# Kernel tuning notes

Measured on AMD Instinct MI355X. Metric: run time of the kernel, lower is better.

Reference implementation:

```python
import jax, jax.numpy as jnp
import numpy as np

N = 50000      # nodes
E = 800000     # edges
IN, HID, OUT = 256, 64, 64
H1, H2 = 4, 1
NEG_SLOPE = 0.2  # DGL GATConv default


def gat_layer(x, W, a_l, a_r, b, src, dst, n_heads, d_out, activation=None):
    # x: [N, F_in]; W: [F_in, n_heads*d_out]; a_l/a_r: [n_heads, d_out]; b: [n_heads*d_out]
    z = (x @ W).reshape(N, n_heads, d_out)                      # [N,H,D]
    el = jnp.sum(z * a_l[None], axis=-1)                        # [N,H] score from src side
    er = jnp.sum(z * a_r[None], axis=-1)                        # [N,H] score from dst side
    e = jax.nn.leaky_relu(el[src] + er[dst], NEG_SLOPE)         # [E,H]
    # edge-softmax normalized over incoming edges of each dst node
    m = jax.ops.segment_max(e, dst, num_segments=N)             # [N,H]
    ex = jnp.exp(e - m[dst])                                    # [E,H]
    s = jax.ops.segment_sum(ex, dst, num_segments=N)            # [N,H]
    alpha = ex / s[dst]                                         # [E,H]
    # scatter-weighted aggregation of neighbor (src) features
    msg = alpha[:, :, None] * z[src]                            # [E,H,D]
    out = jax.ops.segment_sum(msg, dst, num_segments=N)         # [N,H,D]
    out = out + b.reshape(1, n_heads, d_out)
    if activation is not None:
        out = activation(out)
    return out


def setup_inputs() -> dict:
    key = jax.random.key(0)
    ks = jax.random.split(key, 12)
    x = jax.random.normal(ks[0], (N, IN), dtype=jnp.float32)
    src = jax.random.randint(ks[1], (E,), 0, N, dtype=jnp.int32)
    dst = jax.random.randint(ks[2], (E,), 0, N, dtype=jnp.int32)
    sc1 = 1.0 / np.sqrt(IN)
    sc2 = 1.0 / np.sqrt(HID * H1)
    W1 = jax.random.normal(ks[3], (IN, H1 * HID), dtype=jnp.float32) * sc1
    al1 = jax.random.normal(ks[4], (H1, HID), dtype=jnp.float32) * 0.1
    ar1 = jax.random.normal(ks[5], (H1, HID), dtype=jnp.float32) * 0.1
    b1 = jnp.zeros((H1 * HID,), dtype=jnp.float32)
    W2 = jax.random.normal(ks[6], (HID * H1, H2 * OUT), dtype=jnp.float32) * sc2
    al2 = jax.random.normal(ks[7], (H2, OUT), dtype=jnp.float32) * 0.1
    ar2 = jax.random.normal(ks[8], (H2, OUT), dtype=jnp.float32) * 0.1
    b2 = jnp.zeros((H2 * OUT,), dtype=jnp.float32)
    return {"x": x, "W1": W1, "al1": al1, "ar1": ar1, "b1": b1,
            "W2": W2, "al2": al2, "ar2": ar2, "b2": b2,
            "src": src, "dst": dst}


def reference(x, W1, al1, ar1, b1, W2, al2, ar2, b2, src, dst):
    # layer 1: GATConv(IN -> HID, H1 heads), elu activation, then flatten heads
    h = gat_layer(x, W1, al1, ar1, b1, src, dst, H1, HID, activation=jax.nn.elu)
    h = h.reshape(N, H1 * HID)
    # layer 2: GATConv(HID*H1 -> OUT, H2 heads), no activation, mean over heads
    h = gat_layer(h, W2, al2, ar2, b2, src, dst, H2, OUT, activation=None)
    return h.mean(axis=1)  # [N, OUT]
```

## Files before the change

### kernel.cpp

```cpp
#include <hip/hip_runtime.h>
#include <hip/hip_bf16.h>
#include <math.h>

#define NN 50000
#define EE 800000
#define FIN 256
#define HID 64
#define OUTD 64
#define H1 4
#define H2 1

typedef __attribute__((ext_vector_type(8))) short short8;
typedef __attribute__((ext_vector_type(4))) short short4v;
typedef __attribute__((ext_vector_type(4))) float f32x4;
typedef __attribute__((ext_vector_type(2))) float f32x2;


__device__ __forceinline__ unsigned short f2bf(float f) {
    unsigned u = __float_as_uint(f);
    unsigned r = (u + 0x7FFFu + ((u >> 16) & 1u)) >> 16;
    return (unsigned short)r;
}
__device__ __forceinline__ float bf2f(unsigned short u) {
    return __uint_as_float(((unsigned)u) << 16);
}


__global__ void hist_kernel(const int* __restrict__ dst, int* __restrict__ deg, int nE) {
    int e = blockIdx.x * 256 + threadIdx.x;
    if (e < nE) atomicAdd(&deg[dst[e]], 1);
}

__global__ void scan_block(const int* __restrict__ in, int* __restrict__ out,
                           int* __restrict__ bsums, int n) {
    __shared__ int sh[256];
    int i = blockIdx.x * 256 + threadIdx.x;
    int v = (i < n) ? in[i] : 0;
    sh[threadIdx.x] = v;
    __syncthreads();
    for (int off = 1; off < 256; off <<= 1) {
        int t = 0;
        if (threadIdx.x >= off) t = sh[threadIdx.x - off];
        __syncthreads();
        if (threadIdx.x >= off) sh[threadIdx.x] += t;
        __syncthreads();
    }
    if (i < n) out[i] = sh[threadIdx.x] - v;
    if (threadIdx.x == 255) bsums[blockIdx.x] = sh[255];
}

__global__ void scan_bsums(int* __restrict__ bsums, int nb) {
    __shared__ int sh[256];
    int v = (threadIdx.x < nb) ? bsums[threadIdx.x] : 0;
    sh[threadIdx.x] = v;
    __syncthreads();
    for (int off = 1; off < 256; off <<= 1) {
        int t = 0;
        if (threadIdx.x >= off) t = sh[threadIdx.x - off];
        __syncthreads();
        if (threadIdx.x >= off) sh[threadIdx.x] += t;
        __syncthreads();
    }
    if (threadIdx.x < nb) bsums[threadIdx.x] = sh[threadIdx.x] - v;
}

__global__ void add_offsets(int* __restrict__ out, const int* __restrict__ bsums,
                            int n, int Etot) {
    int i = blockIdx.x * 256 + threadIdx.x;
    if (i < n) out[i] += bsums[blockIdx.x];
    if (i == 0) out[n] = Etot;
}

__global__ void fill_csr(const int* __restrict__ src, const int* __restrict__ dst,
                         const int* __restrict__ rowptr, int* __restrict__ fillc,
                         int* __restrict__ csr_src, int nE) {
    int e = blockIdx.x * 256 + threadIdx.x;
    if (e < nE) {
        int d = dst[e];
        int pos = rowptr[d] + atomicAdd(&fillc[d], 1);
        csr_src[pos] = src[e];
    }
}


__global__ void wsplit(const float* __restrict__ W1, const float* __restrict__ W2,
                       short* __restrict__ W1th, short* __restrict__ W1tl,
                       short* __restrict__ W2th, short* __restrict__ W2tl) {
    int n = blockIdx.x;
    int k = threadIdx.x;
    if (n < 256) {
        float v = W1[(size_t)k * 256 + n];
        unsigned short hi = f2bf(v);
        unsigned short lo = f2bf(v - bf2f(hi));
        W1th[n * 256 + k] = (short)hi;
        W1tl[n * 256 + k] = (short)lo;
    } else {
        int n2 = n - 256;
        float v = W2[(size_t)k * 64 + n2];
        unsigned short hi = f2bf(v);
        unsigned short lo = f2bf(v - bf2f(hi));
        W2th[n2 * 256 + k] = (short)hi;
        W2tl[n2 * 256 + k] = (short)lo;
    }
}


template<int MF, int WR, int WC, int NT, int H, bool ASPLIT>
__global__ __launch_bounds__(256) void gemm_bf16x2(
    const void* __restrict__ Av, const short* __restrict__ Bth, const short* __restrict__ Btl,
    const float* __restrict__ al, const float* __restrict__ ar,
    unsigned short* __restrict__ zb, float* __restrict__ el, float* __restrict__ er,
    int M, int K)
{
    constexpr int BM = WR * MF * 16;
    constexpr int BN = WC * 64;
    __shared__ short Ah[BM * 40];
    __shared__ short Al[ASPLIT ? BM * 40 : 8];
    __shared__ short Bh[BN * 40], Bl[BN * 40];

    const int bm = blockIdx.x * BM;
    const int bn = blockIdx.y * BN;
    const int t = threadIdx.x;
    const int wid = t >> 6;
    const int lane = t & 63;
    const int lr = lane & 15;
    const int lg = lane >> 4;
    const int wr = wid / WC;
    const int wc = wid % WC;

    f32x4 acc[MF][4];
#pragma unroll
    for (int mf = 0; mf < MF; ++mf)
#pragma unroll
        for (int nf = 0; nf < 4; ++nf) acc[mf][nf] = (f32x4)(0.f);

    for (int k0 = 0; k0 < K; k0 += 32) {
        if constexpr (ASPLIT) {
            const float* A = (const float*)Av;
#pragma unroll
            for (int q = 0; q < BM / 32; ++q) {
                int linear = q * 256 + t;
                int row = linear >> 3;
                int kq = (linear & 7) * 4;
                int grow = bm + row;
                float4 av = make_float4(0.f, 0.f, 0.f, 0.f);
                if (grow < M) av = *(const float4*)(A + (size_t)grow * K + k0 + kq);
                short4v hi, lo;
                unsigned short h0 = f2bf(av.x); hi.x = (short)h0; lo.x = (short)f2bf(av.x - bf2f(h0));
                unsigned short h1v = f2bf(av.y); hi.y = (short)h1v; lo.y = (short)f2bf(av.y - bf2f(h1v));
                unsigned short h2v = f2bf(av.z); hi.z = (short)h2v; lo.z = (short)f2bf(av.z - bf2f(h2v));
                unsigned short h3v = f2bf(av.w); hi.w = (short)h3v; lo.w = (short)f2bf(av.w - bf2f(h3v));
                *(short4v*)&Ah[row * 40 + kq] = hi;
                *(short4v*)&Al[row * 40 + kq] = lo;
            }
        } else {
            const unsigned short* A = (const unsigned short*)Av;
#pragma unroll
            for (int q = 0; q < BM / 64; ++q) {
                int linear = q * 256 + t;
                int row = linear >> 2;
                int k8 = (linear & 3) * 8;
                int grow = bm + row;
                short8 v = (short8)(0);
                if (grow < M) v = *(const short8*)(A + (size_t)grow * K + k0 + k8);
                *(short8*)&Ah[row * 40 + k8] = v;
            }
        }
#pragma unroll
        for (int q = 0; q < BN / 64; ++q) {
            int linear = q * 256 + t;
            int n = linear >> 2;
            int k8 = (linear & 3) * 8;
            short8 vh = *(const short8*)(Bth + (size_t)(bn + n) * K + k0 + k8);
            short8 vl = *(const short8*)(Btl + (size_t)(bn + n) * K + k0 + k8);
            *(short8*)&Bh[n * 40 + k8] = vh;
            *(short8*)&Bl[n * 40 + k8] = vl;
        }
        __syncthreads();

        short8 ah[MF], alo[MF], bh[4], blo[4];
#pragma unroll
        for (int mf = 0; mf < MF; ++mf) {
            int row = wr * MF * 16 + mf * 16 + lr;
            ah[mf] = *(const short8*)&Ah[row * 40 + lg * 8];
            if constexpr (ASPLIT) alo[mf] = *(const short8*)&Al[row * 40 + lg * 8];
        }
#pragma unroll
        for (int nf = 0; nf < 4; ++nf) {
            int col = wc * 64 + nf * 16 + lr;
            bh[nf]  = *(const short8*)&Bh[col * 40 + lg * 8];
            blo[nf] = *(const short8*)&Bl[col * 40 + lg * 8];
        }
#pragma unroll
        for (int mf = 0; mf < MF; ++mf)
#pragma unroll
            for (int nf = 0; nf < 4; ++nf) {
                acc[mf][nf] = __builtin_amdgcn_mfma_f32_16x16x32_bf16(ah[mf], bh[nf],  acc[mf][nf], 0, 0, 0);
                acc[mf][nf] = __builtin_amdgcn_mfma_f32_16x16x32_bf16(ah[mf], blo[nf], acc[mf][nf], 0, 0, 0);
                if constexpr (ASPLIT)
                    acc[mf][nf] = __builtin_amdgcn_mfma_f32_16x16x32_bf16(alo[mf], bh[nf], acc[mf][nf], 0, 0, 0);
            }
        __syncthreads();
    }

    const int h = (bn + wc * 64) >> 6;
    float alv[4], arv[4];
#pragma unroll
    for (int nf = 0; nf < 4; ++nf) {
        alv[nf] = al[h * 64 + nf * 16 + lr];
        arv[nf] = ar[h * 64 + nf * 16 + lr];
    }
#pragma unroll
    for (int mf = 0; mf < MF; ++mf) {
#pragma unroll
        for (int j = 0; j < 4; ++j) {
            int row = bm + wr * MF * 16 + mf * 16 + lg * 4 + j;
            float sel = 0.f, ser = 0.f;
#pragma unroll
            for (int nf = 0; nf < 4; ++nf) {
                float v = acc[mf][nf][j];
                sel += v * alv[nf];
                ser += v * arv[nf];
                if (row < M)
                    zb[(size_t)row * NT + bn + wc * 64 + nf * 16 + lr] = f2bf(v);
            }
#pragma unroll
            for (int off = 1; off <= 8; off <<= 1) {
                sel += __shfl_xor(sel, off);
                ser += __shfl_xor(ser, off);
            }
            if (lr == 0 && row < M) {
                el[(size_t)row * H + h] = sel;
                er[(size_t)row * H + h] = ser;
            }
        }
    }
}


__global__ __launch_bounds__(256) void gat_aggregate_h4(
    const unsigned short* __restrict__ zb,
    const float* __restrict__ el,
    const float* __restrict__ er,
    const int* __restrict__ rowptr, const int* __restrict__ csr_src,
    const float* __restrict__ bias,
    unsigned short* __restrict__ out,
    int Nn)
{
    __shared__ float p_lds[4][64][4];
    __shared__ int   s_lds[4][64];
    int wid = threadIdx.x >> 6;
    int lane = threadIdx.x & 63;
    int n = blockIdx.x * 4 + wid;
    if (n >= Nn) return;
    int start = rowptr[n], end = rowptr[n + 1];
    int deg = end - start;
    float4 er4 = *(const float4*)(er + (size_t)n * 4);
    int hsel = lane >> 4;
    const unsigned lb = (unsigned)(lane << 3);

    f32x2 acc01 = {0.f, 0.f}, acc23 = {0.f, 0.f};
    float4 ssum = make_float4(0.f, 0.f, 0.f, 0.f);
    float m = -INFINITY;

    for (int c0 = 0; c0 < deg; c0 += 64) {
        int nc = min(64, deg - c0);
        int s_l = 0;
        float4 e4 = make_float4(-INFINITY, -INFINITY, -INFINITY, -INFINITY);
        float emax_l = -INFINITY;
        if (lane < nc) {
            s_l = csr_src[start + c0 + lane];
            float4 el4 = *(const float4*)(el + (size_t)s_l * 4);
            e4.x = el4.x + er4.x; e4.x = e4.x > 0.f ? e4.x : 0.2f * e4.x;
            e4.y = el4.y + er4.y; e4.y = e4.y > 0.f ? e4.y : 0.2f * e4.y;
            e4.z = el4.z + er4.z; e4.z = e4.z > 0.f ? e4.z : 0.2f * e4.z;
            e4.w = el4.w + er4.w; e4.w = e4.w > 0.f ? e4.w : 0.2f * e4.w;
            emax_l = fmaxf(fmaxf(e4.x, e4.y), fmaxf(e4.z, e4.w));
        }
        float cm = emax_l;
#pragma unroll
        for (int off = 32; off; off >>= 1) cm = fmaxf(cm, __shfl_xor(cm, off));
        float newm = fmaxf(m, cm);
        float scale = __expf(m - newm);
        ssum.x *= scale; ssum.y *= scale; ssum.z *= scale; ssum.w *= scale;
        f32x2 sc2 = {scale, scale};
        acc01 *= sc2; acc23 *= sc2;
        m = newm;
        float4 p4 = make_float4(0.f, 0.f, 0.f, 0.f);
        if (lane < nc) {
            p4.x = __expf(e4.x - m);
            p4.y = __expf(e4.y - m);
            p4.z = __expf(e4.z - m);
            p4.w = __expf(e4.w - m);
        }
        float4 cs = p4;
#pragma unroll
        for (int off = 32; off; off >>= 1) {
            cs.x += __shfl_xor(cs.x, off);
            cs.y += __shfl_xor(cs.y, off);
            cs.z += __shfl_xor(cs.z, off);
            cs.w += __shfl_xor(cs.w, off);
        }
        ssum.x += cs.x; ssum.y += cs.y; ssum.z += cs.z; ssum.w += cs.w;
        *(float4*)&p_lds[wid][lane][0] = p4;
        s_lds[wid][lane] = s_l;

        for (int tt = 0; tt < nc; tt += 8) {
            float w[8]; unsigned off32[8];
#pragma unroll
            for (int j = 0; j < 8; ++j) {
                int idx = tt + j;
                int ic = idx < nc ? idx : 0;
                w[j] = idx < nc ? p_lds[wid][ic][hsel] : 0.f;
                off32[j] = ((unsigned)s_lds[wid][ic] << 9) + lb;
            }
            uint2 u[8];
#pragma unroll
            for (int j = 0; j < 8; ++j)
                u[j] = *(const uint2*)((const char*)zb + off32[j]);
#pragma unroll
            for (int j = 0; j < 8; ++j) {
                f32x2 v01, v23, ww = {w[j], w[j]};
                v01.x = __uint_as_float(u[j].x << 16);
                v01.y = __uint_as_float(u[j].x & 0xffff0000u);
                v23.x = __uint_as_float(u[j].y << 16);
                v23.y = __uint_as_float(u[j].y & 0xffff0000u);
                acc01 = __builtin_elementwise_fma(ww, v01, acc01);
                acc23 = __builtin_elementwise_fma(ww, v23, acc23);
            }
        }
    }
    float4 acc = make_float4(acc01.x, acc01.y, acc23.x, acc23.y);
#pragma unroll
    for (int off = 16; off <= 32; off <<= 1) { }
    float s_h = hsel == 0 ? ssum.x : hsel == 1 ? ssum.y : hsel == 2 ? ssum.z : ssum.w;
    float inv = s_h > 0.f ? 1.f / s_h : 0.f;
    float4 b4 = *(const float4*)(bias + lane * 4);
    float ox = acc.x * inv + b4.x; ox = ox > 0.f ? ox : expm1f(ox);
    float oy = acc.y * inv + b4.y; oy = oy > 0.f ? oy : expm1f(oy);
    float oz = acc.z * inv + b4.z; oz = oz > 0.f ? oz : expm1f(oz);
    float ow = acc.w * inv + b4.w; ow = ow > 0.f ? ow : expm1f(ow);
    ushort4 o;
    o.x = f2bf(ox); o.y = f2bf(oy); o.z = f2bf(oz); o.w = f2bf(ow);
    *(ushort4*)(out + (size_t)n * 256 + lane * 4) = o;
}


__global__ void gat_aggregate_bf(const unsigned short* __restrict__ zb,
                                 const float* __restrict__ el, const float* __restrict__ er,
                                 const int* __restrict__ rowptr, const int* __restrict__ csr_src,
                                 const float* __restrict__ bias,
                                 float* __restrict__ out, int Nn)
{
    int gw = (blockIdx.x * blockDim.x + threadIdx.x) >> 6;
    int lane = threadIdx.x & 63;
    int n = gw;
    if (n >= Nn) return;
    int start = rowptr[n], end = rowptr[n + 1];
    int deg = end - start;
    float ern = er[n];

    int group = lane >> 4;
    int gl = lane & 15;
    const unsigned lb = (unsigned)(gl << 3);

    f32x2 acc01 = {0.f, 0.f}, acc23 = {0.f, 0.f};
    float m = -INFINITY;
    float ssum = 0.f;

    for (int c0 = 0; c0 < deg; c0 += 64) {
        int nc = min(64, deg - c0);
        int s_l = 0;
        float e_l = -INFINITY;
        if (lane < nc) {
            s_l = csr_src[start + c0 + lane];
            float e = el[s_l] + ern;
            e_l = e > 0.f ? e : 0.2f * e;
        }
        float cm = e_l;
#pragma unroll
        for (int off = 32; off; off >>= 1) cm = fmaxf(cm, __shfl_xor(cm, off));
        float newm = fmaxf(m, cm);
        float scale = __expf(m - newm);
        ssum *= scale;
        f32x2 sc2 = {scale, scale};
        acc01 *= sc2; acc23 *= sc2;
        m = newm;
        float p_l = (lane < nc) ? __expf(e_l - m) : 0.f;
        float cs = p_l;
#pragma unroll
        for (int off = 32; off; off >>= 1) cs += __shfl_xor(cs, off);
        ssum += cs;

        int nIter = (nc + 3) >> 2;
        for (int i0 = 0; i0 < nIter; i0 += 4) {
            float w[4]; unsigned off32[4];
#pragma unroll
            for (int j = 0; j < 4; ++j) {
                int tt = group + 4 * (i0 + j);
                int tc = tt & 63;
                float wv = __shfl(p_l, tc);
                int s = __shfl(s_l, tc);
                w[j] = (tt < nc) ? wv : 0.f;
                off32[j] = ((unsigned)s << 7) + lb;
            }
            uint2 u[4];
#pragma unroll
            for (int j = 0; j < 4; ++j)
                u[j] = *(const uint2*)((const char*)zb + off32[j]);
#pragma unroll
            for (int j = 0; j < 4; ++j) {
                f32x2 v01, v23, ww = {w[j], w[j]};
                v01.x = __uint_as_float(u[j].x << 16);
                v01.y = __uint_as_float(u[j].x & 0xffff0000u);
                v23.x = __uint_as_float(u[j].y << 16);
                v23.y = __uint_as_float(u[j].y & 0xffff0000u);
                acc01 = __builtin_elementwise_fma(ww, v01, acc01);
                acc23 = __builtin_elementwise_fma(ww, v23, acc23);
            }
        }
    }
    float4 acc = make_float4(acc01.x, acc01.y, acc23.x, acc23.y);
#pragma unroll
    for (int off = 16; off <= 32; off <<= 1) {
        acc.x += __shfl_xor(acc.x, off);
        acc.y += __shfl_xor(acc.y, off);
        acc.z += __shfl_xor(acc.z, off);
        acc.w += __shfl_xor(acc.w, off);
    }
    float inv = ssum > 0.f ? 1.f / ssum : 0.f;
    if (lane < 16) {
        float4 o;
        o.x = acc.x * inv + bias[gl * 4 + 0];
        o.y = acc.y * inv + bias[gl * 4 + 1];
        o.z = acc.z * inv + bias[gl * 4 + 2];
        o.w = acc.w * inv + bias[gl * 4 + 3];
        *(float4*)(out + (size_t)n * 64 + gl * 4) = o;
    }
}


static inline size_t align_up(size_t x, size_t a) { return (x + a - 1) & ~(a - 1); }

extern "C" void kernel_launch(void* const* d_in, const int* in_sizes, int n_in,
                              void* d_out, int out_size, void* d_ws, size_t ws_size,
                              hipStream_t stream) {
    const float* x   = (const float*)d_in[0];
    const float* W1  = (const float*)d_in[1];
    const float* al1 = (const float*)d_in[2];
    const float* ar1 = (const float*)d_in[3];
    const float* b1  = (const float*)d_in[4];
    const float* W2  = (const float*)d_in[5];
    const float* al2 = (const float*)d_in[6];
    const float* ar2 = (const float*)d_in[7];
    const float* b2  = (const float*)d_in[8];
    const int*   src = (const int*)d_in[9];
    const int*   dst = (const int*)d_in[10];
    float* out = (float*)d_out;

    char* ws = (char*)d_ws;
    size_t off = 0;
    unsigned short* zb1 = (unsigned short*)(ws + off); off = align_up(off + (size_t)NN * 256 * 2, 256);
    unsigned short* h1b = (unsigned short*)(ws + off); off = align_up(off + (size_t)NN * 256 * 2, 256);
    unsigned short* zb2 = (unsigned short*)(ws + off); off = align_up(off + (size_t)NN * 64 * 2, 256);
    float* el1 = (float*)(ws + off); off = align_up(off + (size_t)NN * H1 * 4, 256);
    float* er1 = (float*)(ws + off); off = align_up(off + (size_t)NN * H1 * 4, 256);
    float* el2 = (float*)(ws + off); off = align_up(off + (size_t)NN * 4, 256);
    float* er2 = (float*)(ws + off); off = align_up(off + (size_t)NN * 4, 256);
    short* W1th = (short*)(ws + off); off = align_up(off + 256 * 256 * 2, 256);
    short* W1tl = (short*)(ws + off); off = align_up(off + 256 * 256 * 2, 256);
    short* W2th = (short*)(ws + off); off = align_up(off + 64 * 256 * 2, 256);
    short* W2tl = (short*)(ws + off); off = align_up(off + 64 * 256 * 2, 256);
    int* rowptr = (int*)(ws + off); off = align_up(off + (size_t)(NN + 1) * 4, 256);
    int* deg    = (int*)(ws + off); off = align_up(off + (size_t)NN * 4, 256);
    int* fillc  = (int*)(ws + off); off = align_up(off + (size_t)NN * 4, 256);
    int* bsums  = (int*)(ws + off); off = align_up(off + 256 * 4, 256);
    int* csr_src = (int*)(ws + off); off = align_up(off + (size_t)EE * 4, 256);

    const int nScanBlocks = (NN + 255) / 256;
    const int nEdgeBlocks = (EE + 255) / 256;
    const int nMBlocks64 = (NN + 63) / 64;
    const int nMBlocks128 = (NN + 127) / 128;

    hipMemsetAsync(deg, 0, (size_t)NN * 4, stream);
    hipMemsetAsync(fillc, 0, (size_t)NN * 4, stream);
    wsplit<<<320, 256, 0, stream>>>(W1, W2, W1th, W1tl, W2th, W2tl);
    hist_kernel<<<nEdgeBlocks, 256, 0, stream>>>(dst, deg, EE);
    scan_block<<<nScanBlocks, 256, 0, stream>>>(deg, rowptr, bsums, NN);
    scan_bsums<<<1, 256, 0, stream>>>(bsums, nScanBlocks);
    add_offsets<<<nScanBlocks, 256, 0, stream>>>(rowptr, bsums, NN, EE);
    fill_csr<<<nEdgeBlocks, 256, 0, stream>>>(src, dst, rowptr, fillc, csr_src, EE);

    gemm_bf16x2<4, 1, 4, 256, 4, true><<<dim3(nMBlocks64, 1), 256, 0, stream>>>(
        x, W1th, W1tl, al1, ar1, zb1, el1, er1, NN, FIN);
    gat_aggregate_h4<<<(NN + 3) / 4, 256, 0, stream>>>(
        zb1, el1, er1, rowptr, csr_src, b1, h1b, NN);

    gemm_bf16x2<2, 4, 1, 64, 1, false><<<dim3(nMBlocks128, 1), 256, 0, stream>>>(
        h1b, W2th, W2tl, al2, ar2, zb2, el2, er2, NN, H1 * HID);
    gat_aggregate_bf<<<(NN * 64 + 255) / 256, 256, 0, stream>>>(
        zb2, el2, er2, rowptr, csr_src, b2, out, NN);
}
```

Baseline: 244.4 us.

## Fuse weight split into histogram, single-block scan, and enlarge layer-1 GEMM tile

Merges the weight bf16 hi/lo split into the edge-degree histogram kernel and replaces the three-kernel block scan with one 1024-thread single-block scan, cutting the number of launches in CSR construction. The layer-1 GEMM tile grows from 64 to 128 rows per block, and A fragments are loaded inside the mf loop so more rows fit without keeping every fragment live in registers. The single-block scan serialises 50k elements onto one CU, and the bigger GEMM tile halves the block count and may raise register pressure.

```diff
diff --git a/kernel.cpp b/kernel.cpp
--- a/kernel.cpp
+++ b/kernel.cpp
@@ -26,49 +26,67 @@
 }
 
 
-__global__ void hist_kernel(const int* __restrict__ dst, int* __restrict__ deg, int nE) {
+__global__ void hist_wsplit(const int* __restrict__ dst, int* __restrict__ deg, int nE,
+                            const float* __restrict__ W1, const float* __restrict__ W2,
+                            short* __restrict__ W1th, short* __restrict__ W1tl,
+                            short* __restrict__ W2th, short* __restrict__ W2tl) {
     int e = blockIdx.x * 256 + threadIdx.x;
     if (e < nE) atomicAdd(&deg[dst[e]], 1);
-}
-
-__global__ void scan_block(const int* __restrict__ in, int* __restrict__ out,
-                           int* __restrict__ bsums, int n) {
-    __shared__ int sh[256];
-    int i = blockIdx.x * 256 + threadIdx.x;
-    int v = (i < n) ? in[i] : 0;
-    sh[threadIdx.x] = v;
+    int n = blockIdx.x;
+    int k = threadIdx.x;
+    if (n < 256) {
+        float v = W1[(size_t)k * 256 + n];
+        unsigned short hi = f2bf(v);
+        unsigned short lo = f2bf(v - bf2f(hi));
+        W1th[n * 256 + k] = (short)hi;
+        W1tl[n * 256 + k] = (short)lo;
+    } else if (n < 320) {
+        int n2 = n - 256;
+        float v = W2[(size_t)k * 64 + n2];
+        unsigned short hi = f2bf(v);
+        unsigned short lo = f2bf(v - bf2f(hi));
+        W2th[n2 * 256 + k] = (short)hi;
+        W2tl[n2 * 256 + k] = (short)lo;
+    }
+}
+
+#define SCAN_CH 49
+__global__ __launch_bounds__(1024) void scan_one(const int* __restrict__ deg,
+                                                 int* __restrict__ rowptr) {
+    __shared__ int wsum[16];
+    int tid = threadIdx.x;
+    int lane = tid & 63;
+    int base = tid * SCAN_CH;
+    int loc[SCAN_CH];
+    int tot = 0;
+#pragma unroll
+    for (int j = 0; j < SCAN_CH; ++j) {
+        int idx = base + j;
+        int v = (idx < NN) ? deg[idx] : 0;
+        loc[j] = tot;
+        tot += v;
+    }
+    int incl = tot;
+#pragma unroll
+    for (int off = 1; off < 64; off <<= 1) {
+        int t = __shfl_up(incl, off);
+        if (lane >= off) incl += t;
+    }
+    if (lane == 63) wsum[tid >> 6] = incl;
     __syncthreads();
-    for (int off = 1; off < 256; off <<= 1) {
-        int t = 0;
-        if (threadIdx.x >= off) t = sh[threadIdx.x - off];
-        __syncthreads();
-        if (threadIdx.x >= off) sh[threadIdx.x] += t;
-        __syncthreads();
-    }
-    if (i < n) out[i] = sh[threadIdx.x] - v;
-    if (threadIdx.x == 255) bsums[blockIdx.x] = sh[255];
-}
-
-__global__ void scan_bsums(int* __restrict__ bsums, int nb) {
-    __shared__ int sh[256];
-    int v = (threadIdx.x < nb) ? bsums[threadIdx.x] : 0;
-    sh[threadIdx.x] = v;
+    if (tid == 0) {
+        int run = 0;
+#pragma unroll
+        for (int i = 0; i < 16; ++i) { int t = wsum[i]; wsum[i] = run; run += t; }
+    }
     __syncthreads();
-    for (int off = 1; off < 256; off <<= 1) {
-        int t = 0;
-        if (threadIdx.x >= off) t = sh[threadIdx.x - off];
-        __syncthreads();
-        if (threadIdx.x >= off) sh[threadIdx.x] += t;
-        __syncthreads();
-    }
-    if (threadIdx.x < nb) bsums[threadIdx.x] = sh[threadIdx.x] - v;
-}
-
-__global__ void add_offsets(int* __restrict__ out, const int* __restrict__ bsums,
-                            int n, int Etot) {
-    int i = blockIdx.x * 256 + threadIdx.x;
-    if (i < n) out[i] += bsums[blockIdx.x];
-    if (i == 0) out[n] = Etot;
+    int excl = wsum[tid >> 6] + incl - tot;
+#pragma unroll
+    for (int j = 0; j < SCAN_CH; ++j) {
+        int idx = base + j;
+        if (idx < NN) rowptr[idx] = excl + loc[j];
+    }
+    if (tid == 0) rowptr[NN] = EE;
 }
 
 __global__ void fill_csr(const int* __restrict__ src, const int* __restrict__ dst,
@@ -79,28 +97,6 @@
         int d = dst[e];
         int pos = rowptr[d] + atomicAdd(&fillc[d], 1);
         csr_src[pos] = src[e];
-    }
-}
-
-
-__global__ void wsplit(const float* __restrict__ W1, const float* __restrict__ W2,
-                       short* __restrict__ W1th, short* __restrict__ W1tl,
-                       short* __restrict__ W2th, short* __restrict__ W2tl) {
-    int n = blockIdx.x;
-    int k = threadIdx.x;
-    if (n < 256) {
-        float v = W1[(size_t)k * 256 + n];
-        unsigned short hi = f2bf(v);
-        unsigned short lo = f2bf(v - bf2f(hi));
-        W1th[n * 256 + k] = (short)hi;
-        W1tl[n * 256 + k] = (short)lo;
-    } else {
-        int n2 = n - 256;
-        float v = W2[(size_t)k * 64 + n2];
-        unsigned short hi = f2bf(v);
-        unsigned short lo = f2bf(v - bf2f(hi));
-        W2th[n2 * 256 + k] = (short)hi;
-        W2tl[n2 * 256 + k] = (short)lo;
     }
 }
 
@@ -178,13 +174,7 @@
         }
         __syncthreads();
 
-        short8 ah[MF], alo[MF], bh[4], blo[4];
-#pragma unroll
-        for (int mf = 0; mf < MF; ++mf) {
-            int row = wr * MF * 16 + mf * 16 + lr;
-            ah[mf] = *(const short8*)&Ah[row * 40 + lg * 8];
-            if constexpr (ASPLIT) alo[mf] = *(const short8*)&Al[row * 40 + lg * 8];
-        }
+        short8 bh[4], blo[4];
 #pragma unroll
         for (int nf = 0; nf < 4; ++nf) {
             int col = wc * 64 + nf * 16 + lr;
@@ -192,14 +182,19 @@
             blo[nf] = *(const short8*)&Bl[col * 40 + lg * 8];
         }
 #pragma unroll
-        for (int mf = 0; mf < MF; ++mf)
+        for (int mf = 0; mf < MF; ++mf) {
+            int row = wr * MF * 16 + mf * 16 + lr;
+            short8 ah = *(const short8*)&Ah[row * 40 + lg * 8];
+            short8 alo;
+            if constexpr (ASPLIT) alo = *(const short8*)&Al[row * 40 + lg * 8];
 #pragma unroll
             for (int nf = 0; nf < 4; ++nf) {
-                acc[mf][nf] = __builtin_amdgcn_mfma_f32_16x16x32_bf16(ah[mf], bh[nf],  acc[mf][nf], 0, 0, 0);
-                acc[mf][nf] = __builtin_amdgcn_mfma_f32_16x16x32_bf16(ah[mf], blo[nf], acc[mf][nf], 0, 0, 0);
+                acc[mf][nf] = __builtin_amdgcn_mfma_f32_16x16x32_bf16(ah, bh[nf],  acc[mf][nf], 0, 0, 0);
+                acc[mf][nf] = __builtin_amdgcn_mfma_f32_16x16x32_bf16(ah, blo[nf], acc[mf][nf], 0, 0, 0);
                 if constexpr (ASPLIT)
-                    acc[mf][nf] = __builtin_amdgcn_mfma_f32_16x16x32_bf16(alo[mf], bh[nf], acc[mf][nf], 0, 0, 0);
-            }
+                    acc[mf][nf] = __builtin_amdgcn_mfma_f32_16x16x32_bf16(alo, bh[nf], acc[mf][nf], 0, 0, 0);
+            }
+        }
         __syncthreads();
     }
 
@@ -331,8 +326,6 @@
         }
     }
     float4 acc = make_float4(acc01.x, acc01.y, acc23.x, acc23.y);
-#pragma unroll
-    for (int off = 16; off <= 32; off <<= 1) { }
     float s_h = hsel == 0 ? ssum.x : hsel == 1 ? ssum.y : hsel == 2 ? ssum.z : ssum.w;
     float inv = s_h > 0.f ? 1.f / s_h : 0.f;
     float4 b4 = *(const float4*)(bias + lane * 4);
@@ -474,24 +467,18 @@
     int* rowptr = (int*)(ws + off); off = align_up(off + (size_t)(NN + 1) * 4, 256);
     int* deg    = (int*)(ws + off); off = align_up(off + (size_t)NN * 4, 256);
     int* fillc  = (int*)(ws + off); off = align_up(off + (size_t)NN * 4, 256);
-    int* bsums  = (int*)(ws + off); off = align_up(off + 256 * 4, 256);
     int* csr_src = (int*)(ws + off); off = align_up(off + (size_t)EE * 4, 256);
 
-    const int nScanBlocks = (NN + 255) / 256;
     const int nEdgeBlocks = (EE + 255) / 256;
-    const int nMBlocks64 = (NN + 63) / 64;
     const int nMBlocks128 = (NN + 127) / 128;
 
     hipMemsetAsync(deg, 0, (size_t)NN * 4, stream);
     hipMemsetAsync(fillc, 0, (size_t)NN * 4, stream);
-    wsplit<<<320, 256, 0, stream>>>(W1, W2, W1th, W1tl, W2th, W2tl);
-    hist_kernel<<<nEdgeBlocks, 256, 0, stream>>>(dst, deg, EE);
-    scan_block<<<nScanBlocks, 256, 0, stream>>>(deg, rowptr, bsums, NN);
-    scan_bsums<<<1, 256, 0, stream>>>(bsums, nScanBlocks);
-    add_offsets<<<nScanBlocks, 256, 0, stream>>>(rowptr, bsums, NN, EE);
+    hist_wsplit<<<nEdgeBlocks, 256, 0, stream>>>(dst, deg, EE, W1, W2, W1th, W1tl, W2th, W2tl);
+    scan_one<<<1, 1024, 0, stream>>>(deg, rowptr);
     fill_csr<<<nEdgeBlocks, 256, 0, stream>>>(src, dst, rowptr, fillc, csr_src, EE);
 
-    gemm_bf16x2<4, 1, 4, 256, 4, true><<<dim3(nMBlocks64, 1), 256, 0, stream>>>(
+    gemm_bf16x2<8, 1, 4, 256, 4, true><<<dim3(nMBlocks128, 1), 256, 0, stream>>>(
         x, W1th, W1tl, al1, ar1, zb1, el1, er1, NN, FIN);
     gat_aggregate_h4<<<(NN + 3) / 4, 256, 0, stream>>>(
         zb1, el1, er1, rowptr, csr_src, b1, h1b, NN);
```

Result: slower. 314.9 us (+28.9%).
